# Optimization experiments

Hardware: AMD Instinct MI355X
Metric: run time of the kernel (lower is better)

The kernel has to match this reference:

```python
import jax, jax.numpy as jnp
import numpy as np

N = 100_000            # nodes
E = 1_600_000          # edges (avg degree 16)
IN, OUT = 64, 16
L1, L2 = 48, 32        # in - floor(k*(in-out)/3) for k=1,2
EDGE_DIM = 16
EPS = 1e-7             # GENConv message epsilon
BN_EPS = 1e-5


def _lin(k, i, o):
    return jax.random.normal(k, (i, o), jnp.float32) / np.float32(np.sqrt(i))


def setup_inputs() -> dict:
    key = jax.random.key(0)
    ks = jax.random.split(key, 16)
    z = lambda d: jnp.zeros((d,), jnp.float32)
    o = lambda d: jnp.ones((d,), jnp.float32)
    return {
        "x": jax.random.normal(ks[0], (N, IN), jnp.float32),
        "edge_index": jax.random.randint(ks[1], (2, E), 0, N),
        "edge_attr": jax.random.normal(ks[2], (E, EDGE_DIM), jnp.float32),
        # GENConv 1 (IN -> L1)
        "w_src1": _lin(ks[3], IN, L1), "b_src1": z(L1),
        "w_edge1": _lin(ks[4], EDGE_DIM, L1), "b_edge1": z(L1),
        "w_m1a": _lin(ks[5], L1, 2 * L1), "b_m1a": z(2 * L1),
        "g1": o(2 * L1), "be1": z(2 * L1),
        "w_m1b": _lin(ks[6], 2 * L1, L1), "b_m1b": z(L1),
        # GENConv 2 (L1 -> L2)
        "w_src2": _lin(ks[7], L1, L2), "b_src2": z(L2),
        "w_edge2": _lin(ks[8], EDGE_DIM, L2), "b_edge2": z(L2),
        "w_m2a": _lin(ks[9], L2, 2 * L2), "b_m2a": z(2 * L2),
        "g2": o(2 * L2), "be2": z(2 * L2),
        "w_m2b": _lin(ks[10], 2 * L2, L2), "b_m2b": z(L2),
        # GCNConv heads (L2 -> OUT)
        "w_mu": _lin(ks[11], L2, OUT), "b_mu": z(OUT),
        "w_ls": _lin(ks[12], L2, OUT), "b_ls": z(OUT),
    }


def _gen_conv(x, src, dst, e_raw, w_src, b_src, w_edge, b_edge,
              w1, b1, g, be, w2, b2):
    """PyG GENConv with softmax aggregation (t=1) and 2-layer MLP w/ batch norm."""
    h = x @ w_src + b_src                      # [N, d] lin_src
    e = e_raw @ w_edge + b_edge                # [E, d] lin_edge
    msg = jax.nn.relu(h[src] + e) + EPS        # [E, d] message
    # per-destination, per-channel softmax aggregation
    mmax = jax.ops.segment_max(msg, dst, num_segments=N)
    mmax = jnp.where(jnp.isfinite(mmax), mmax, 0.0)
    ex = jnp.exp(msg - mmax[dst])
    denom = jax.ops.segment_sum(ex, dst, num_segments=N)
    agg = jax.ops.segment_sum(ex * msg, dst, num_segments=N) / (denom + 1e-16)
    out = agg + h                              # residual with x_dst (lin_src applied)
    # MLP: Linear -> BatchNorm(train stats) -> ReLU -> Linear
    zt = out @ w1 + b1
    zt = (zt - zt.mean(0)) * jax.lax.rsqrt(zt.var(0) + BN_EPS) * g + be
    return jax.nn.relu(zt) @ w2 + b2


def _gcn_conv(x, src, dst, w, b):
    """PyG GCNConv: self-loops + symmetric normalization."""
    loop = jnp.arange(N)
    s = jnp.concatenate([src, loop])
    d = jnp.concatenate([dst, loop])
    deg = jax.ops.segment_sum(jnp.ones(s.shape, x.dtype), d, num_segments=N)
    dinv = jnp.where(deg > 0, jax.lax.rsqrt(deg), 0.0)
    norm = (dinv[s] * dinv[d])[:, None]
    return jax.ops.segment_sum((x @ w)[s] * norm, d, num_segments=N) + b


def reference(x, edge_index, edge_attr,
              w_src1, b_src1, w_edge1, b_edge1, w_m1a, b_m1a, g1, be1, w_m1b, b_m1b,
              w_src2, b_src2, w_edge2, b_edge2, w_m2a, b_m2a, g2, be2, w_m2b, b_m2b,
              w_mu, b_mu, w_ls, b_ls):
    src, dst = edge_index[0], edge_index[1]
    h = jax.nn.relu(_gen_conv(x, src, dst, edge_attr, w_src1, b_src1, w_edge1,
                              b_edge1, w_m1a, b_m1a, g1, be1, w_m1b, b_m1b))
    h = jax.nn.relu(_gen_conv(h, src, dst, edge_attr, w_src2, b_src2, w_edge2,
                              b_edge2, w_m2a, b_m2a, g2, be2, w_m2b, b_m2b))
    mu = _gcn_conv(h, src, dst, w_mu, b_mu)
    logstd = _gcn_conv(h, src, dst, w_ls, b_ls)
    return (mu, logstd)
```

## Files before the change

kernel.cpp:

```cpp
#include <hip/hip_runtime.h>
#include <hip/hip_bf16.h>

typedef unsigned int u32;
typedef unsigned short u16;
typedef _Float16 h2 __attribute__((ext_vector_type(2)));

#define EPS_MSG 1e-7f
#define BN_EPS  1e-5f

__device__ __forceinline__ u16 f2bf(float f) {
  u32 u = __float_as_uint(f);
  return (u16)((u + 0x7FFFu + ((u >> 16) & 1u)) >> 16);
}
__device__ __forceinline__ float bf1(u16 v) { return __uint_as_float(((u32)v) << 16); }
__device__ __forceinline__ h2 u2h(u32 v) { union { u32 u; h2 h; } t; t.u = v; return t.h; }

__device__ __forceinline__ u32 pkrtz(float a, float b) {
  union { __fp16 v __attribute__((ext_vector_type(2))); u32 u; } t;
  t.v = __builtin_amdgcn_cvt_pkrtz(a, b);
  return t.u;
}

__device__ __forceinline__ float dot8(uint4 v, const u32* w, float acc) {
  acc = __builtin_amdgcn_fdot2(u2h(v.x), u2h(w[0]), acc, false);
  acc = __builtin_amdgcn_fdot2(u2h(v.y), u2h(w[1]), acc, false);
  acc = __builtin_amdgcn_fdot2(u2h(v.z), u2h(w[2]), acc, false);
  acc = __builtin_amdgcn_fdot2(u2h(v.w), u2h(w[3]), acc, false);
  return acc;
}

#define EDGE_DOT(A0,A1,A2,A3) (bias + \
  A0.x * wc[0]  + A0.y * wc[1]  + A0.z * wc[2]  + A0.w * wc[3] + \
  A1.x * wc[4]  + A1.y * wc[5]  + A1.z * wc[6]  + A1.w * wc[7] + \
  A2.x * wc[8]  + A2.y * wc[9]  + A2.z * wc[10] + A2.w * wc[11] + \
  A3.x * wc[12] + A3.y * wc[13] + A3.z * wc[14] + A3.w * wc[15])

template<int I, int O, bool WBF>
__global__ void k_lin(const float* __restrict__ X, const float* __restrict__ W,
                      const float* __restrict__ B, float* __restrict__ Y,
                      u16* __restrict__ Ybf, int ldY, int n) {
  __shared__ float Wl[I * O];
  __shared__ float Bl[O];
  for (int t = threadIdx.x; t < I * O; t += blockDim.x) Wl[t] = W[t];
  if (threadIdx.x < O) Bl[threadIdx.x] = B[threadIdx.x];
  __syncthreads();
  int i = blockIdx.x * blockDim.x + threadIdx.x;
  if (i >= n) return;
  float acc[O];
#pragma unroll
  for (int c = 0; c < O; c++) acc[c] = Bl[c];
  const float4* xp = (const float4*)(X + (size_t)i * I);
  for (int q = 0; q < I / 4; q++) {
    float4 v = xp[q];
#pragma unroll
    for (int c = 0; c < O; c++) acc[c] += v.x * Wl[(4 * q + 0) * O + c];
#pragma unroll
    for (int c = 0; c < O; c++) acc[c] += v.y * Wl[(4 * q + 1) * O + c];
#pragma unroll
    for (int c = 0; c < O; c++) acc[c] += v.z * Wl[(4 * q + 2) * O + c];
#pragma unroll
    for (int c = 0; c < O; c++) acc[c] += v.w * Wl[(4 * q + 3) * O + c];
  }
  float* y = Y + (size_t)i * ldY;
#pragma unroll
  for (int c = 0; c < O; c++) y[c] = acc[c];
  if (WBF) {
    u16* yb = Ybf + (size_t)i * O;
#pragma unroll
    for (int c = 0; c < O; c++) yb[c] = f2bf(acc[c]);
  }
}

__global__ void k_deg(const int* __restrict__ ei, u32* __restrict__ deg, int E) {
  int e = blockIdx.x * blockDim.x + threadIdx.x;
  if (e < E) atomicAdd(&deg[ei[E + e]], 1u);
}

__global__ void k_scan1(const u32* __restrict__ deg, u32* __restrict__ excl,
                        u32* __restrict__ part, int n) {
  __shared__ u32 sm[256];
  int t = threadIdx.x;
  int base = blockIdx.x * 1024 + t * 4;
  u32 v0 = (base + 0 < n) ? deg[base + 0] : 0u;
  u32 v1 = (base + 1 < n) ? deg[base + 1] : 0u;
  u32 v2 = (base + 2 < n) ? deg[base + 2] : 0u;
  u32 v3 = (base + 3 < n) ? deg[base + 3] : 0u;
  u32 tsum = v0 + v1 + v2 + v3;
  sm[t] = tsum;
  __syncthreads();
  for (int o = 1; o < 256; o <<= 1) {
    u32 v = (t >= o) ? sm[t - o] : 0u;
    __syncthreads();
    sm[t] += v;
    __syncthreads();
  }
  u32 tex = sm[t] - tsum;
  if (t == 255) part[blockIdx.x] = sm[255];
  if (base + 0 < n) excl[base + 0] = tex;
  if (base + 1 < n) excl[base + 1] = tex + v0;
  if (base + 2 < n) excl[base + 2] = tex + v0 + v1;
  if (base + 3 < n) excl[base + 3] = tex + v0 + v1 + v2;
}

__global__ void k_scan2(u32* __restrict__ part, int nb) {
  if (threadIdx.x == 0) {
    u32 acc = 0;
    for (int i = 0; i < nb; i++) { u32 v = part[i]; part[i] = acc; acc += v; }
  }
}

__global__ void k_scan3(u32* __restrict__ rowptr, const u32* __restrict__ part,
                        const u32* __restrict__ deg, float* __restrict__ dinv,
                        int n, int E) {
  int i = blockIdx.x * blockDim.x + threadIdx.x;
  if (i < n) {
    rowptr[i] += part[i >> 10];
    dinv[i] = rsqrtf((float)(deg[i] + 1u));
  }
  if (i == 0) rowptr[n] = (u32)E;
}

__global__ void k_slots(const int* __restrict__ ei, const u32* __restrict__ rowptr,
                        u32* __restrict__ cnt, int* __restrict__ csr_src,
                        int* __restrict__ csr_eid, int E) {
  int e = blockIdx.x * blockDim.x + threadIdx.x;
  if (e >= E) return;
  int s = ei[e], d = ei[E + e];
  u32 slot = rowptr[d] + atomicAdd(&cnt[d], 1u);
  csr_src[slot] = s;
  csr_eid[slot] = e;
}

__global__ void k_gather(const int* __restrict__ csr_eid, const float* __restrict__ ea,
                         u32* __restrict__ eaperm, int E) {
  int i = blockIdx.x * blockDim.x + threadIdx.x;
  if (i >= E) return;
  int e = csr_eid[i];
  const float4* p = (const float4*)(ea + (size_t)e * 16);
  float4 a = p[0], b = p[1], c = p[2], d = p[3];
  uint4* q = (uint4*)(eaperm + (size_t)i * 8);
  uint4 w0, w1;
  w0.x = pkrtz(a.x, a.y);
  w0.y = pkrtz(a.z, a.w);
  w0.z = pkrtz(b.x, b.y);
  w0.w = pkrtz(b.z, b.w);
  w1.x = pkrtz(c.x, c.y);
  w1.y = pkrtz(c.z, c.w);
  w1.z = pkrtz(d.x, d.y);
  w1.w = pkrtz(d.z, d.w);
  q[0] = w0; q[1] = w1;
}

template<bool PERM>
__global__ void k_agg48(const u32* __restrict__ rowptr, const int* __restrict__ csr_src,
                        const int* __restrict__ csr_eid, const u32* __restrict__ eaperm,
                        const float* __restrict__ ea,
                        const float* __restrict__ we, const float* __restrict__ be,
                        const float* __restrict__ h, const u16* __restrict__ hbf,
                        float* __restrict__ out, int n) {
  int lane = threadIdx.x & 63;
  int cl   = (lane < 48) ? lane : lane - 48;
  int node = (blockIdx.x * blockDim.x + threadIdx.x) >> 6;
  if (node >= n) return;
  float bias = be[cl];
  float hself = h[(size_t)node * 48 + cl];
  u32 b = rowptr[node], t = rowptr[node + 1];
  float den = 0.f, num = 0.f;
  u32 i = b;
  if (PERM) {
    u32 wcp[8];
#pragma unroll
    for (int k = 0; k < 8; k++)
      wcp[k] = pkrtz(we[(2 * k + 0) * 48 + cl], we[(2 * k + 1) * 48 + cl]);
    for (; i + 2 <= t; i += 2) {
      int s0 = csr_src[i + 0];
      int s1 = csr_src[i + 1];
      const uint4* pa = (const uint4*)(eaperm + (size_t)i * 8);
      uint4 a0 = pa[0], a1 = pa[1];
      uint4 b0 = pa[2], b1 = pa[3];
      float h0 = bf1(hbf[(size_t)s0 * 48 + cl]);
      float h1 = bf1(hbf[(size_t)s1 * 48 + cl]);
      float ml0 = dot8(a1, wcp + 4, dot8(a0, wcp, bias));
      float ml1 = dot8(b1, wcp + 4, dot8(b0, wcp, bias));
      float m0 = fmaxf(h0 + ml0, 0.f) + EPS_MSG;
      float m1 = fmaxf(h1 + ml1, 0.f) + EPS_MSG;
      float ex0 = __expf(m0);
      float ex1 = __expf(m1);
      den += ex0 + ex1;
      num += ex0 * m0 + ex1 * m1;
    }
    for (; i < t; i++) {
      int s = csr_src[i];
      const uint4* pa = (const uint4*)(eaperm + (size_t)i * 8);
      uint4 a0 = pa[0], a1 = pa[1];
      float hv = bf1(hbf[(size_t)s * 48 + cl]);
      float ml = dot8(a1, wcp + 4, dot8(a0, wcp, bias));
      float m  = fmaxf(hv + ml, 0.f) + EPS_MSG;
      float ex = __expf(m);
      den += ex; num += ex * m;
    }
  } else {
    float wc[16];
#pragma unroll
    for (int k = 0; k < 16; k++) wc[k] = we[k * 48 + cl];
    for (; i < t; i++) {
      int s = csr_src[i];
      const float4* p = (const float4*)(ea + (size_t)csr_eid[i] * 16);
      float4 a0 = p[0], a1 = p[1], a2 = p[2], a3 = p[3];
      float hv = h[(size_t)s * 48 + cl];
      float ml = EDGE_DOT(a0, a1, a2, a3);
      float m  = fmaxf(hv + ml, 0.f) + EPS_MSG;
      float ex = __expf(m);
      den += ex; num += ex * m;
    }
  }
  if (lane < 48)
    out[(size_t)node * 48 + lane] = hself + num / (den + 1e-16f);
}

template<bool PERM>
__global__ void k_agg32(const u32* __restrict__ rowptr, const int* __restrict__ csr_src,
                        const int* __restrict__ csr_eid, const u32* __restrict__ eaperm,
                        const float* __restrict__ ea,
                        const float* __restrict__ we, const float* __restrict__ be,
                        const float* __restrict__ h, const u16* __restrict__ hbf,
                        float* __restrict__ out, int n) {
  int c    = threadIdx.x & 31;
  int node = (blockIdx.x * blockDim.x + threadIdx.x) >> 5;
  if (node >= n) return;
  float bias = be[c];
  float hself = h[(size_t)node * 32 + c];
  u32 b = rowptr[node], t = rowptr[node + 1];
  float den = 0.f, num = 0.f;
  u32 i = b;
  if (PERM) {
    u32 wcp[8];
#pragma unroll
    for (int k = 0; k < 8; k++)
      wcp[k] = pkrtz(we[(2 * k + 0) * 32 + c], we[(2 * k + 1) * 32 + c]);
    for (; i + 2 <= t; i += 2) {
      int s0 = csr_src[i + 0];
      int s1 = csr_src[i + 1];
      const uint4* pa = (const uint4*)(eaperm + (size_t)i * 8);
      uint4 a0 = pa[0], a1 = pa[1];
      uint4 b0 = pa[2], b1 = pa[3];
      float h0 = bf1(hbf[(size_t)s0 * 32 + c]);
      float h1 = bf1(hbf[(size_t)s1 * 32 + c]);
      float ml0 = dot8(a1, wcp + 4, dot8(a0, wcp, bias));
      float ml1 = dot8(b1, wcp + 4, dot8(b0, wcp, bias));
      float m0 = fmaxf(h0 + ml0, 0.f) + EPS_MSG;
      float m1 = fmaxf(h1 + ml1, 0.f) + EPS_MSG;
      float ex0 = __expf(m0);
      float ex1 = __expf(m1);
      den += ex0 + ex1;
      num += ex0 * m0 + ex1 * m1;
    }
    for (; i < t; i++) {
      int s = csr_src[i];
      const uint4* pa = (const uint4*)(eaperm + (size_t)i * 8);
      uint4 a0 = pa[0], a1 = pa[1];
      float hv = bf1(hbf[(size_t)s * 32 + c]);
      float ml = dot8(a1, wcp + 4, dot8(a0, wcp, bias));
      float m  = fmaxf(hv + ml, 0.f) + EPS_MSG;
      float ex = __expf(m);
      den += ex; num += ex * m;
    }
  } else {
    float wc[16];
#pragma unroll
    for (int k = 0; k < 16; k++) wc[k] = we[k * 32 + c];
    for (; i < t; i++) {
      int s = csr_src[i];
      const float4* p = (const float4*)(ea + (size_t)csr_eid[i] * 16);
      float4 a0 = p[0], a1 = p[1], a2 = p[2], a3 = p[3];
      float hv = h[(size_t)s * 32 + c];
      float ml = EDGE_DOT(a0, a1, a2, a3);
      float m  = fmaxf(hv + ml, 0.f) + EPS_MSG;
      float ex = __expf(m);
      den += ex; num += ex * m;
    }
  }
  out[(size_t)node * 32 + c] = hself + num / (den + 1e-16f);
}

template<int D>
__global__ void k_ztstats(const float* __restrict__ X, const float* __restrict__ W,
                          const float* __restrict__ B, float* __restrict__ Z1,
                          float* __restrict__ Z2, float* __restrict__ partial, int n) {
  __shared__ float Wl[D * 2 * D];
  __shared__ float Bl[2 * D];
  __shared__ float red[4][4 * D];
  for (int t = threadIdx.x; t < D * 2 * D; t += blockDim.x) Wl[t] = W[t];
  for (int t = threadIdx.x; t < 2 * D; t += blockDim.x) Bl[t] = B[t];
  __syncthreads();
  int i = blockIdx.x * blockDim.x + threadIdx.x;
  bool act = (i < n);
  float acc[2 * D];
#pragma unroll
  for (int c = 0; c < 2 * D; c++) acc[c] = 0.f;
  if (act) {
#pragma unroll
    for (int c = 0; c < 2 * D; c++) acc[c] = Bl[c];
    const float4* xp = (const float4*)(X + (size_t)i * D);
    for (int q = 0; q < D / 4; q++) {
      float4 v = xp[q];
#pragma unroll
      for (int c = 0; c < 2 * D; c++) acc[c] += v.x * Wl[(4 * q + 0) * 2 * D + c];
#pragma unroll
      for (int c = 0; c < 2 * D; c++) acc[c] += v.y * Wl[(4 * q + 1) * 2 * D + c];
#pragma unroll
      for (int c = 0; c < 2 * D; c++) acc[c] += v.z * Wl[(4 * q + 2) * 2 * D + c];
#pragma unroll
      for (int c = 0; c < 2 * D; c++) acc[c] += v.w * Wl[(4 * q + 3) * 2 * D + c];
    }
    float* z1 = Z1 + (size_t)i * D;
    float* z2 = Z2 + (size_t)i * D;
#pragma unroll
    for (int c = 0; c < D; c++) { z1[c] = acc[c]; z2[c] = acc[D + c]; }
  } else {
#pragma unroll
    for (int c = 0; c < 2 * D; c++) acc[c] = 0.f;
  }
  int lane = threadIdx.x & 63;
  int wv   = threadIdx.x >> 6;
#pragma unroll
  for (int c = 0; c < 2 * D; c++) {
    float v = acc[c], v2 = v * v;
#pragma unroll
    for (int o = 32; o; o >>= 1) { v += __shfl_xor(v, o); v2 += __shfl_xor(v2, o); }
    if (lane == 0) { red[wv][c] = v; red[wv][2 * D + c] = v2; }
  }
  __syncthreads();
  if (threadIdx.x < 4 * D) {
    float s = red[0][threadIdx.x] + red[1][threadIdx.x] +
              red[2][threadIdx.x] + red[3][threadIdx.x];
    partial[(size_t)blockIdx.x * 4 * D + threadIdx.x] = s;
  }
}

__global__ void k_bnfin(const float* __restrict__ partial, float* __restrict__ stats,
                        int nb, int m) {
  int c = blockIdx.x * blockDim.x + threadIdx.x;
  if (c >= m) return;
  float s = 0.f;
  for (int b = 0; b < nb; b++) s += partial[(size_t)b * m + c];
  stats[c] = s;
}

template<int D, int DD, int O, bool ADDBS, bool WBF, bool SCALE>
__global__ void k_mlp_lin(const float* __restrict__ ztA, const float* __restrict__ ztB,
                          const float* __restrict__ stats,
                          const float* __restrict__ G, const float* __restrict__ BE,
                          const float* __restrict__ W2, const float* __restrict__ B2,
                          const float* __restrict__ Wsa, const float* __restrict__ Wsb,
                          const float* __restrict__ Bs, const float* __restrict__ dinv,
                          float* __restrict__ out, u16* __restrict__ outbf,
                          float invN, int n) {
  __shared__ float Wl[DD * D];
  __shared__ float Ws[D * O];
  __shared__ float Bl[D];
  __shared__ float Bsl[O];
  __shared__ float sc[DD], sh[DD];
  for (int t = threadIdx.x; t < DD * D; t += blockDim.x) Wl[t] = W2[t];
  if (Wsb == nullptr) {
    for (int t = threadIdx.x; t < D * O; t += blockDim.x) Ws[t] = Wsa[t];
  } else {
    for (int t = threadIdx.x; t < D * O; t += blockDim.x) {
      int k = t / O, o = t % O;
      Ws[t] = (o < O / 2) ? Wsa[k * (O / 2) + o] : Wsb[k * (O / 2) + (o - O / 2)];
    }
  }
  if (threadIdx.x < D) Bl[threadIdx.x] = B2[threadIdx.x];
  if (threadIdx.x < O) Bsl[threadIdx.x] = ADDBS ? Bs[threadIdx.x] : 0.f;
  if (threadIdx.x < DD) {
    int c   = threadIdx.x;
    float m = stats[c] * invN;
    float v = stats[DD + c] * invN - m * m;
    float s = G[c] * rsqrtf(v + BN_EPS);
    sc[c] = s; sh[c] = BE[c] - m * s;
  }
  __syncthreads();
  int i = blockIdx.x * blockDim.x + threadIdx.x;
  if (i >= n) return;
  float y[D];
#pragma unroll
  for (int c = 0; c < D; c++) y[c] = Bl[c];
  const float* a = ztA + (size_t)i * D;
  const float* b = ztB + (size_t)i * D;
  for (int k = 0; k < D; k++) {
    float z = fmaxf(a[k] * sc[k] + sh[k], 0.f);
#pragma unroll
    for (int c = 0; c < D; c++) y[c] += z * Wl[k * D + c];
  }
  for (int k = D; k < DD; k++) {
    float z = fmaxf(b[k - D] * sc[k] + sh[k], 0.f);
#pragma unroll
    for (int c = 0; c < D; c++) y[c] += z * Wl[k * D + c];
  }
  float acc[O];
#pragma unroll
  for (int o = 0; o < O; o++) acc[o] = Bsl[o];
#pragma unroll
  for (int k = 0; k < D; k++) {
    float z = fmaxf(y[k], 0.f);
#pragma unroll
    for (int o = 0; o < O; o++) acc[o] += z * Ws[k * O + o];
  }
  float dv = SCALE ? dinv[i] : 1.f;
  float* yo = out + (size_t)i * O;
#pragma unroll
  for (int o = 0; o < O; o++) yo[o] = SCALE ? acc[o] * dv : acc[o];
  if (WBF) {
    u16* yb = outbf + (size_t)i * O;
#pragma unroll
    for (int o = 0; o < O; o++) yb[o] = f2bf(acc[o]);
  }
}

__global__ void k_gcn(const u32* __restrict__ rowptr, const int* __restrict__ csr_src,
                      const float* __restrict__ yzd, const float* __restrict__ dinv,
                      const float* __restrict__ bmu, const float* __restrict__ bls,
                      float* __restrict__ out, int n) {
  int c    = threadIdx.x & 31;
  int node = (blockIdx.x * blockDim.x + threadIdx.x) >> 5;
  if (node >= n) return;
  u32 b = rowptr[node], t = rowptr[node + 1];
  float acc = 0.f;
  u32 i = b;
  for (; i + 2 <= t; i += 2) {
    int s0 = csr_src[i];
    int s1 = csr_src[i + 1];
    float y0 = yzd[(size_t)s0 * 32 + c];
    float y1 = yzd[(size_t)s1 * 32 + c];
    acc += y0 + y1;
  }
  if (i < t) acc += yzd[(size_t)csr_src[i] * 32 + c];
  float dv  = dinv[node];
  float val = (acc + yzd[(size_t)node * 32 + c]) * dv +
              ((c < 16) ? bmu[c] : bls[c - 16]);
  if (c < 16) out[(size_t)node * 16 + c] = val;
  else        out[(size_t)n * 16 + (size_t)node * 16 + (c - 16)] = val;
}

extern "C" void kernel_launch(void* const* d_in, const int* in_sizes, int n_in,
                              void* d_out, int out_size, void* d_ws, size_t ws_size,
                              hipStream_t stream) {
  const float* x      = (const float*)d_in[0];
  const int*  ei      = (const int*)d_in[1];
  const float* ea     = (const float*)d_in[2];
  const float* w_src1 = (const float*)d_in[3];  const float* b_src1 = (const float*)d_in[4];
  const float* w_edge1= (const float*)d_in[5];  const float* b_edge1= (const float*)d_in[6];
  const float* w_m1a  = (const float*)d_in[7];  const float* b_m1a  = (const float*)d_in[8];
  const float* g1     = (const float*)d_in[9];  const float* be1    = (const float*)d_in[10];
  const float* w_m1b  = (const float*)d_in[11]; const float* b_m1b  = (const float*)d_in[12];
  const float* w_src2 = (const float*)d_in[13]; const float* b_src2 = (const float*)d_in[14];
  const float* w_edge2= (const float*)d_in[15]; const float* b_edge2= (const float*)d_in[16];
  const float* w_m2a  = (const float*)d_in[17]; const float* b_m2a  = (const float*)d_in[18];
  const float* g2     = (const float*)d_in[19]; const float* be2    = (const float*)d_in[20];
  const float* w_m2b  = (const float*)d_in[21]; const float* b_m2b  = (const float*)d_in[22];
  const float* w_mu   = (const float*)d_in[23]; const float* b_mu   = (const float*)d_in[24];
  const float* w_ls   = (const float*)d_in[25]; const float* b_ls   = (const float*)d_in[26];

  const int N = in_sizes[0] / 64;
  const int E = in_sizes[1] / 2;

  const int NB  = (N + 255) / 256;
  const int EB  = (E + 255) / 256;
  const int SB1 = (N + 1023) / 1024;

  float* ws     = (float*)d_ws;
  size_t N48    = (size_t)N * 48;
  float* P0     = ws;
  float* P1     = ws + N48;
  float* P2     = ws + 2 * N48;
  float* P3     = ws + 3 * N48;
  size_t o      = 4 * N48;
  u32*  rowptr  = (u32*)(ws + o);
  u32*  cnt     = rowptr + (N + 1);
  u32*  deg     = cnt + N;
  u32*  part    = deg + N;
  float* dinv   = (float*)(part + 256);
  float* stats  = dinv + N;
  size_t po     = o + 4 * (size_t)N + 769;
  float* partial= ws + po;
  size_t co     = (po + (size_t)NB * 192 + 3) & ~(size_t)3;
  int*  csr_src = (int*)(ws + co);
  int*  csr_eid = csr_src + E;
  size_t eo     = co + 2 * (size_t)E;
  u32*  eaperm  = (u32*)(ws + eo);
  size_t ho     = eo + 8 * (size_t)E;
  u16*  hbf1    = (u16*)(ws + ho);
  size_t h2o    = ho + 24 * (size_t)N;
  u16*  hbf2    = (u16*)(ws + h2o);
  size_t needB  = (h2o + 16 * (size_t)N + 16) * sizeof(float);
  const bool PERM = (ws_size >= needB);

  dim3 b256(256);

  hipMemsetAsync(cnt, 0, 2 * (size_t)N * sizeof(u32), stream);

  k_deg<<<EB, b256, 0, stream>>>(ei, deg, E);
  k_scan1<<<SB1, b256, 0, stream>>>(deg, rowptr, part, N);
  k_scan2<<<1, 64, 0, stream>>>(part, SB1);
  k_scan3<<<NB, b256, 0, stream>>>(rowptr, part, deg, dinv, N, E);
  k_slots<<<EB, b256, 0, stream>>>(ei, rowptr, cnt, csr_src, csr_eid, E);
  if (PERM) k_gather<<<EB, b256, 0, stream>>>(csr_eid, ea, eaperm, E);

  if (PERM) k_lin<64, 48, true><<<NB, b256, 0, stream>>>(x, w_src1, b_src1, P0, hbf1, 48, N);
  else      k_lin<64, 48, false><<<NB, b256, 0, stream>>>(x, w_src1, b_src1, P0, nullptr, 48, N);
  if (PERM) k_agg48<true><<<(N * 64 + 255) / 256, b256, 0, stream>>>(rowptr, csr_src,
                       csr_eid, eaperm, ea, w_edge1, b_edge1, P0, hbf1, P3, N);
  else      k_agg48<false><<<(N * 64 + 255) / 256, b256, 0, stream>>>(rowptr, csr_src,
                       csr_eid, eaperm, ea, w_edge1, b_edge1, P0, hbf1, P3, N);
  k_ztstats<48><<<NB, b256, 0, stream>>>(P3, w_m1a, b_m1a, P1, P2, partial, N);
  k_bnfin<<<1, 256, 0, stream>>>(partial, stats, NB, 192);
  if (PERM)
    k_mlp_lin<48, 96, 32, true, true, false><<<NB, b256, 0, stream>>>(P1, P2, stats, g1, be1,
                       w_m1b, b_m1b, w_src2, nullptr, b_src2, nullptr, P0, hbf2,
                       1.0f / (float)N, N);
  else
    k_mlp_lin<48, 96, 32, true, false, false><<<NB, b256, 0, stream>>>(P1, P2, stats, g1, be1,
                       w_m1b, b_m1b, w_src2, nullptr, b_src2, nullptr, P0, nullptr,
                       1.0f / (float)N, N);

  if (PERM) k_agg32<true><<<(N * 32 + 255) / 256, b256, 0, stream>>>(rowptr, csr_src,
                       csr_eid, eaperm, ea, w_edge2, b_edge2, P0, hbf2, P3, N);
  else      k_agg32<false><<<(N * 32 + 255) / 256, b256, 0, stream>>>(rowptr, csr_src,
                       csr_eid, eaperm, ea, w_edge2, b_edge2, P0, hbf2, P3, N);
  k_ztstats<32><<<NB, b256, 0, stream>>>(P3, w_m2a, b_m2a, P1, P2, partial, N);
  k_bnfin<<<1, 256, 0, stream>>>(partial, stats + 256, NB, 128);
  k_mlp_lin<32, 64, 32, false, false, true><<<NB, b256, 0, stream>>>(P1, P2, stats + 256,
                       g2, be2, w_m2b, b_m2b, w_mu, w_ls, nullptr, dinv, P0, nullptr,
                       1.0f / (float)N, N);

  k_gcn<<<(N * 32 + 255) / 256, b256, 0, stream>>>(rowptr, csr_src, P0, dinv,
                                                   b_mu, b_ls, (float*)d_out, N);
}
```

Baseline: 936.0 us.

## Preload CSR indices cooperatively per wavefront and gather GCN features in bf16

New measurement: 898.1 us. 4.1% less time.

```diff
diff --git a/kernel.cpp b/kernel.cpp
--- a/kernel.cpp
+++ b/kernel.cpp
@@ -165,21 +165,24 @@
   float bias = be[cl];
   float hself = h[(size_t)node * 48 + cl];
   u32 b = rowptr[node], t = rowptr[node + 1];
+  u32 dn = t - b;
   float den = 0.f, num = 0.f;
-  u32 i = b;
   if (PERM) {
     u32 wcp[8];
 #pragma unroll
     for (int k = 0; k < 8; k++)
       wcp[k] = pkrtz(we[(2 * k + 0) * 48 + cl], we[(2 * k + 1) * 48 + cl]);
-    for (; i + 2 <= t; i += 2) {
-      int s0 = csr_src[i + 0];
-      int s1 = csr_src[i + 1];
-      const uint4* pa = (const uint4*)(eaperm + (size_t)i * 8);
+    u32 nf = dn < 64u ? dn : 64u;
+    int vcsr = ((u32)lane < nf) ? csr_src[b + lane] : 0;
+    u32 j = 0;
+    for (; j + 2 <= nf; j += 2) {
+      int s0 = __builtin_amdgcn_readlane(vcsr, j);
+      int s1 = __builtin_amdgcn_readlane(vcsr, j + 1);
+      float h0 = bf1(hbf[(size_t)s0 * 48 + cl]);
+      float h1 = bf1(hbf[(size_t)s1 * 48 + cl]);
+      const uint4* pa = (const uint4*)(eaperm + (size_t)(b + j) * 8);
       uint4 a0 = pa[0], a1 = pa[1];
       uint4 b0 = pa[2], b1 = pa[3];
-      float h0 = bf1(hbf[(size_t)s0 * 48 + cl]);
-      float h1 = bf1(hbf[(size_t)s1 * 48 + cl]);
       float ml0 = dot8(a1, wcp + 4, dot8(a0, wcp, bias));
       float ml1 = dot8(b1, wcp + 4, dot8(b0, wcp, bias));
       float m0 = fmaxf(h0 + ml0, 0.f) + EPS_MSG;
@@ -189,7 +192,17 @@
       den += ex0 + ex1;
       num += ex0 * m0 + ex1 * m1;
     }
-    for (; i < t; i++) {
+    for (; j < nf; j++) {
+      int s = __builtin_amdgcn_readlane(vcsr, j);
+      const uint4* pa = (const uint4*)(eaperm + (size_t)(b + j) * 8);
+      uint4 a0 = pa[0], a1 = pa[1];
+      float hv = bf1(hbf[(size_t)s * 48 + cl]);
+      float ml = dot8(a1, wcp + 4, dot8(a0, wcp, bias));
+      float m  = fmaxf(hv + ml, 0.f) + EPS_MSG;
+      float ex = __expf(m);
+      den += ex; num += ex * m;
+    }
+    for (u32 i = b + nf; i < t; i++) {
       int s = csr_src[i];
       const uint4* pa = (const uint4*)(eaperm + (size_t)i * 8);
       uint4 a0 = pa[0], a1 = pa[1];
@@ -203,7 +216,7 @@
     float wc[16];
 #pragma unroll
     for (int k = 0; k < 16; k++) wc[k] = we[k * 48 + cl];
-    for (; i < t; i++) {
+    for (u32 i = b; i < t; i++) {
       int s = csr_src[i];
       const float4* p = (const float4*)(ea + (size_t)csr_eid[i] * 16);
       float4 a0 = p[0], a1 = p[1], a2 = p[2], a3 = p[3];
@@ -225,27 +238,33 @@
                         const float* __restrict__ we, const float* __restrict__ be,
                         const float* __restrict__ h, const u16* __restrict__ hbf,
                         float* __restrict__ out, int n) {
-  int c    = threadIdx.x & 31;
+  int lane = threadIdx.x & 63;
+  int c    = lane & 31;
+  int half = (lane >> 5) & 1;
   int node = (blockIdx.x * blockDim.x + threadIdx.x) >> 5;
   if (node >= n) return;
   float bias = be[c];
   float hself = h[(size_t)node * 32 + c];
   u32 b = rowptr[node], t = rowptr[node + 1];
+  u32 dn = t - b;
   float den = 0.f, num = 0.f;
-  u32 i = b;
   if (PERM) {
     u32 wcp[8];
 #pragma unroll
     for (int k = 0; k < 8; k++)
       wcp[k] = pkrtz(we[(2 * k + 0) * 32 + c], we[(2 * k + 1) * 32 + c]);
-    for (; i + 2 <= t; i += 2) {
-      int s0 = csr_src[i + 0];
-      int s1 = csr_src[i + 1];
-      const uint4* pa = (const uint4*)(eaperm + (size_t)i * 8);
+    u32 nf = dn < 32u ? dn : 32u;
+    int vcsr = ((u32)c < nf) ? csr_src[b + c] : 0;
+    int lbase = half << 5;
+    u32 j = 0;
+    for (; j + 2 <= nf; j += 2) {
+      int s0 = __shfl(vcsr, lbase + (int)j);
+      int s1 = __shfl(vcsr, lbase + (int)j + 1);
+      float h0 = bf1(hbf[(size_t)s0 * 32 + c]);
+      float h1 = bf1(hbf[(size_t)s1 * 32 + c]);
+      const uint4* pa = (const uint4*)(eaperm + (size_t)(b + j) * 8);
       uint4 a0 = pa[0], a1 = pa[1];
       uint4 b0 = pa[2], b1 = pa[3];
-      float h0 = bf1(hbf[(size_t)s0 * 32 + c]);
-      float h1 = bf1(hbf[(size_t)s1 * 32 + c]);
       float ml0 = dot8(a1, wcp + 4, dot8(a0, wcp, bias));
       float ml1 = dot8(b1, wcp + 4, dot8(b0, wcp, bias));
       float m0 = fmaxf(h0 + ml0, 0.f) + EPS_MSG;
@@ -255,7 +274,17 @@
       den += ex0 + ex1;
       num += ex0 * m0 + ex1 * m1;
     }
-    for (; i < t; i++) {
+    for (; j < nf; j++) {
+      int s = __shfl(vcsr, lbase + (int)j);
+      const uint4* pa = (const uint4*)(eaperm + (size_t)(b + j) * 8);
+      uint4 a0 = pa[0], a1 = pa[1];
+      float hv = bf1(hbf[(size_t)s * 32 + c]);
+      float ml = dot8(a1, wcp + 4, dot8(a0, wcp, bias));
+      float m  = fmaxf(hv + ml, 0.f) + EPS_MSG;
+      float ex = __expf(m);
+      den += ex; num += ex * m;
+    }
+    for (u32 i = b + nf; i < t; i++) {
       int s = csr_src[i];
       const uint4* pa = (const uint4*)(eaperm + (size_t)i * 8);
       uint4 a0 = pa[0], a1 = pa[1];
@@ -269,7 +298,7 @@
     float wc[16];
 #pragma unroll
     for (int k = 0; k < 16; k++) wc[k] = we[k * 32 + c];
-    for (; i < t; i++) {
+    for (u32 i = b; i < t; i++) {
       int s = csr_src[i];
       const float4* p = (const float4*)(ea + (size_t)csr_eid[i] * 16);
       float4 a0 = p[0], a1 = p[1], a2 = p[2], a3 = p[3];
@@ -347,7 +376,7 @@
   stats[c] = s;
 }
 
-template<int D, int DD, int O, bool ADDBS, bool WBF, bool SCALE>
+template<int D, int DD, int O, bool ADDBS, bool WBF, bool SCALE, bool WOUT>
 __global__ void k_mlp_lin(const float* __restrict__ ztA, const float* __restrict__ ztB,
                           const float* __restrict__ stats,
                           const float* __restrict__ G, const float* __restrict__ BE,
@@ -407,36 +436,48 @@
     for (int o = 0; o < O; o++) acc[o] += z * Ws[k * O + o];
   }
   float dv = SCALE ? dinv[i] : 1.f;
-  float* yo = out + (size_t)i * O;
-#pragma unroll
-  for (int o = 0; o < O; o++) yo[o] = SCALE ? acc[o] * dv : acc[o];
+  if (WOUT) {
+    float* yo = out + (size_t)i * O;
+#pragma unroll
+    for (int o = 0; o < O; o++) yo[o] = SCALE ? acc[o] * dv : acc[o];
+  }
   if (WBF) {
     u16* yb = outbf + (size_t)i * O;
 #pragma unroll
-    for (int o = 0; o < O; o++) yb[o] = f2bf(acc[o]);
+    for (int o = 0; o < O; o++) yb[o] = f2bf(SCALE ? acc[o] * dv : acc[o]);
   }
 }
 
 __global__ void k_gcn(const u32* __restrict__ rowptr, const int* __restrict__ csr_src,
-                      const float* __restrict__ yzd, const float* __restrict__ dinv,
+                      const u16* __restrict__ yzbf, const float* __restrict__ dinv,
                       const float* __restrict__ bmu, const float* __restrict__ bls,
                       float* __restrict__ out, int n) {
-  int c    = threadIdx.x & 31;
+  int lane = threadIdx.x & 63;
+  int c    = lane & 31;
+  int half = (lane >> 5) & 1;
   int node = (blockIdx.x * blockDim.x + threadIdx.x) >> 5;
   if (node >= n) return;
   u32 b = rowptr[node], t = rowptr[node + 1];
+  u32 dn = t - b;
+  u32 nf = dn < 32u ? dn : 32u;
+  int vcsr = ((u32)c < nf) ? csr_src[b + c] : 0;
+  int lbase = half << 5;
   float acc = 0.f;
-  u32 i = b;
-  for (; i + 2 <= t; i += 2) {
-    int s0 = csr_src[i];
-    int s1 = csr_src[i + 1];
-    float y0 = yzd[(size_t)s0 * 32 + c];
-    float y1 = yzd[(size_t)s1 * 32 + c];
+  u32 j = 0;
+  for (; j + 2 <= nf; j += 2) {
+    int s0 = __shfl(vcsr, lbase + (int)j);
+    int s1 = __shfl(vcsr, lbase + (int)j + 1);
+    float y0 = bf1(yzbf[(size_t)s0 * 32 + c]);
+    float y1 = bf1(yzbf[(size_t)s1 * 32 + c]);
     acc += y0 + y1;
   }
-  if (i < t) acc += yzd[(size_t)csr_src[i] * 32 + c];
+  for (; j < nf; j++) {
+    int s = __shfl(vcsr, lbase + (int)j);
+    acc += bf1(yzbf[(size_t)s * 32 + c]);
+  }
+  for (u32 i = b + nf; i < t; i++) acc += bf1(yzbf[(size_t)csr_src[i] * 32 + c]);
   float dv  = dinv[node];
-  float val = (acc + yzd[(size_t)node * 32 + c]) * dv +
+  float val = (acc + bf1(yzbf[(size_t)node * 32 + c])) * dv +
               ((c < 16) ? bmu[c] : bls[c - 16]);
   if (c < 16) out[(size_t)node * 16 + c] = val;
   else        out[(size_t)n * 16 + (size_t)node * 16 + (c - 16)] = val;
@@ -515,12 +556,12 @@
   k_ztstats<48><<<NB, b256, 0, stream>>>(P3, w_m1a, b_m1a, P1, P2, partial, N);
   k_bnfin<<<1, 256, 0, stream>>>(partial, stats, NB, 192);
   if (PERM)
-    k_mlp_lin<48, 96, 32, true, true, false><<<NB, b256, 0, stream>>>(P1, P2, stats, g1, be1,
-                       w_m1b, b_m1b, w_src2, nullptr, b_src2, nullptr, P0, hbf2,
+    k_mlp_lin<48, 96, 32, true, true, false, true><<<NB, b256, 0, stream>>>(P1, P2, stats,
+                       g1, be1, w_m1b, b_m1b, w_src2, nullptr, b_src2, nullptr, P0, hbf2,
                        1.0f / (float)N, N);
   else
-    k_mlp_lin<48, 96, 32, true, false, false><<<NB, b256, 0, stream>>>(P1, P2, stats, g1, be1,
-                       w_m1b, b_m1b, w_src2, nullptr, b_src2, nullptr, P0, nullptr,
+    k_mlp_lin<48, 96, 32, true, false, false, true><<<NB, b256, 0, stream>>>(P1, P2, stats,
+                       g1, be1, w_m1b, b_m1b, w_src2, nullptr, b_src2, nullptr, P0, nullptr,
                        1.0f / (float)N, N);
 
   if (PERM) k_agg32<true><<<(N * 32 + 255) / 256, b256, 0, stream>>>(rowptr, csr_src,
@@ -529,10 +570,10 @@
                        csr_eid, eaperm, ea, w_edge2, b_edge2, P0, hbf2, P3, N);
   k_ztstats<32><<<NB, b256, 0, stream>>>(P3, w_m2a, b_m2a, P1, P2, partial, N);
   k_bnfin<<<1, 256, 0, stream>>>(partial, stats + 256, NB, 128);
-  k_mlp_lin<32, 64, 32, false, false, true><<<NB, b256, 0, stream>>>(P1, P2, stats + 256,
-                       g2, be2, w_m2b, b_m2b, w_mu, w_ls, nullptr, dinv, P0, nullptr,
-                       1.0f / (float)N, N);
-
-  k_gcn<<<(N * 32 + 255) / 256, b256, 0, stream>>>(rowptr, csr_src, P0, dinv,
+  k_mlp_lin<32, 64, 32, false, true, true, false><<<NB, b256, 0, stream>>>(P1, P2,
+                       stats + 256, g2, be2, w_m2b, b_m2b, w_mu, w_ls, nullptr, dinv,
+                       nullptr, hbf2, 1.0f / (float)N, N);
+
+  k_gcn<<<(N * 32 + 255) / 256, b256, 0, stream>>>(rowptr, csr_src, hbf2, dinv,
                                                    b_mu, b_ls, (float*)d_out, N);
 }
```
